# Optimization experiments

Hardware: AMD Instinct MI355X
Metric: run time of the kernel (lower is better)

The kernel has to match this reference:

```python
import jax, jax.numpy as jnp
import numpy as np

S = 4  # MC samples


def _gat_layer(x, mask, w, a_src, a_dst, bias):
    # x: (b,n,fin)  w: (H,fin,fout)  mask: (b,n,n) bool
    h = jnp.einsum('bnf,hfo->bhno', x, w)                      # (b,H,n,fout)
    th = jnp.tanh(h)
    att_src = jnp.einsum('bhno,ho->bhn', th, a_src)
    att_dst = jnp.einsum('bhno,ho->bhn', th, a_dst)
    logits = jax.nn.leaky_relu(att_src[:, :, :, None] + att_dst[:, :, None, :], 0.2)
    logits = jnp.where(mask[:, None, :, :], logits, jnp.float32(-1e9))
    att = jax.nn.softmax(logits, axis=-1)                      # (b,H,n,n)
    out = jnp.einsum('bhij,bhjo->bhio', att, h) + bias         # (b,H,n,fout)
    return out, att


def setup_inputs() -> dict:
    key = jax.random.key(0)
    ks = jax.random.split(key, 11)
    b, n, f0, emb_d = 128, 128, 64, 64
    H1, f1, H2, f2 = 8, 16, 1, 2
    fin1 = f0 + emb_d            # 128 (n_units[0] += 64)
    fin2 = H1 * f1               # 128 (heads concatenated between layers)
    x = jax.random.normal(ks[0], (b, n, f0), jnp.float32)
    emb = jax.random.normal(ks[1], (b, n, emb_d), jnp.float32)
    adj = jax.random.randint(ks[2], (b, n, n), 0, 2).astype(jnp.int32)
    adj = jnp.maximum(adj, jnp.eye(n, dtype=jnp.int32)[None])  # self-loops keep softmax rows valid
    w1 = jax.random.normal(ks[3], (S, H1, fin1, f1), jnp.float32) * 0.1
    a_src1 = jax.random.normal(ks[4], (S, H1, f1), jnp.float32) * 0.1
    a_dst1 = jax.random.normal(ks[5], (S, H1, f1), jnp.float32) * 0.1
    b1 = jax.random.normal(ks[6], (f1,), jnp.float32) * 0.1
    w2 = jax.random.normal(ks[7], (S, H2, fin2, f2), jnp.float32) * 0.1
    a_src2 = jax.random.normal(ks[8], (S, H2, f2), jnp.float32) * 0.1
    a_dst2 = jax.random.normal(ks[9], (S, H2, f2), jnp.float32) * 0.1
    b2 = jax.random.normal(ks[10], (f2,), jnp.float32) * 0.1
    return dict(x=x, emb=emb, adj=adj, w1=w1, a_src1=a_src1, a_dst1=a_dst1, b1=b1,
                w2=w2, a_src2=a_src2, a_dst2=a_dst2, b2=b2)


def reference(x, emb, adj, w1, a_src1, a_dst1, b1, w2, a_src2, a_dst2, b2):
    mask = adj.astype(bool)
    x0 = jnp.concatenate([x, emb], axis=-1)                    # (b,n,128)
    b, n = x0.shape[0], x0.shape[1]
    xs = jnp.broadcast_to(x0, (S,) + x0.shape)                 # same input for each MC sample
    layer = jax.vmap(_gat_layer, in_axes=(0, None, 0, 0, 0, None))
    # layer 1 (per-sample variational weights), ELU activation
    h1, att1 = layer(xs, mask, w1, a_src1, a_dst1, b1)         # h1: (S,b,H1,n,f1)
    h1 = jax.nn.elu(h1)
    # concat heads: transpose(1,2).view(bs,n,-1)
    xs2 = jnp.transpose(h1, (0, 1, 3, 2, 4)).reshape(S, b, n, -1)
    # layer 2 (last layer): no activation, mean over heads
    h2, att2 = layer(xs2, mask, w2, a_src2, a_dst2, b2)        # (S,b,1,n,2)
    out = h2.mean(axis=2)                                      # (S,b,n,2)
    logp = jax.nn.log_softmax(out, axis=-1)[:, :, -1, :]       # (S,b,2) -> ego node
    result = jnp.mean(logp, axis=0)                            # var_mean -> mean (return_uncertainty=False)
    return result
```

## Files before the change

### kernel.cpp

```cpp
#include <hip/hip_runtime.h>
#include <stdint.h>
#include <math.h>

typedef __attribute__((ext_vector_type(8))) short short8;
typedef __attribute__((ext_vector_type(4))) float floatx4;

#define L_HF    0
#define L_SRC   16384
#define L_DST   18432
#define L_MASK  20480
#define L_H2P   22528
#define L_SIZE  26624

union F8 { short8 s8; uint32_t u[4]; };

#if __has_builtin(__builtin_amdgcn_exp2f)
#define EXP2F __builtin_amdgcn_exp2f
#else
#define EXP2F exp2f
#endif
#define LOG2E 1.4426950408889634f

__device__ __forceinline__ uint32_t packbf(float a, float b){
  uint32_t ua = __float_as_uint(a), ub = __float_as_uint(b);
  uint32_t ra = (ua + 0x7fffu + ((ua>>16)&1u)) >> 16;
  uint32_t rb = (ub + 0x7fffu + ((ub>>16)&1u)) >> 16;
  return ra | (rb<<16);
}
__device__ __forceinline__ uint32_t packbf_t(float a, float b){
  return __builtin_amdgcn_perm(__float_as_uint(b), __float_as_uint(a), 0x07060302u);
}
__device__ __forceinline__ float fast_tanh(float x){
  float e = __expf(2.f*x);
  return 1.f - 2.f*__builtin_amdgcn_rcpf(e + 1.f);
}
__device__ __forceinline__ float red16(float x){
  x += __int_as_float(__builtin_amdgcn_update_dpp(0, __float_as_int(x), 0x128, 0xf, 0xf, true));
  x += __int_as_float(__builtin_amdgcn_update_dpp(0, __float_as_int(x), 0x124, 0xf, 0xf, true));
  x += __int_as_float(__builtin_amdgcn_update_dpp(0, __float_as_int(x), 0x122, 0xf, 0xf, true));
  x += __int_as_float(__builtin_amdgcn_update_dpp(0, __float_as_int(x), 0x121, 0xf, 0xf, true));
  return x;
}

__global__ __launch_bounds__(512,8) void gat_fused(
    const float* __restrict__ x,  const float* __restrict__ emb,
    const int* __restrict__ adj,  const float* __restrict__ w1,
    const float* __restrict__ a_src1, const float* __restrict__ a_dst1,
    const float* __restrict__ b1, const float* __restrict__ w2,
    float* __restrict__ ws_h2)
{
  __shared__ __align__(16) char smem[L_SIZE];
  char*     hf    = smem + L_HF;
  uint32_t* hf_u  = (uint32_t*)(smem + L_HF);
  float*    src_l = (float*)(smem + L_SRC);
  float*    dst_l = (float*)(smem + L_DST);
  uint32_t* mask_l= (uint32_t*)(smem + L_MASK);
  const uint4* mask4 = (const uint4*)(smem + L_MASK);
  float2*   h2p   = (float2*)(smem + L_H2P);

  const int t    = threadIdx.x;
  const int blk  = blockIdx.x;
  const int s    = blk >> 8;
  const int bb   = (blk & 255) >> 1;
  const int half = blk & 1;
  const int lane = t & 63, w = t >> 6;
  const int of = lane & 15, kg = lane >> 4;

  const int arow = w*16 + of;
  const float* xrow = x   + ((size_t)bb*128 + arow)*64;
  const float* erow = emb + ((size_t)bb*128 + arow)*64;
  short8 af[4];
  #pragma unroll
  for (int ks=0; ks<4; ++ks){
    int k = ks*32 + kg*8;
    const float* p = (k<64) ? (xrow+k) : (erow + (k-64));
    float4 f0 = *(const float4*)p, f1 = *(const float4*)(p+4);
    F8 fr;
    fr.u[0]=packbf(f0.x,f0.y); fr.u[1]=packbf(f0.z,f0.w);
    fr.u[2]=packbf(f1.x,f1.y); fr.u[3]=packbf(f1.z,f1.w);
    af[ks]=fr.s8;
  }

  {
    const float* w1s = w1 + (size_t)s*16384 + half*8192;
    #pragma unroll
    for (int r=0; r<2; ++r){
      int q = t + r*512;
      int ql = q & 63, ks = (q>>6)&3, ct = q>>8;
      const float* wp = w1s + ct*2048 + (ks*32 + (ql>>4)*8)*16 + (ql&15);
      F8 fr;
      fr.u[0]=packbf(wp[0],  wp[16]);
      fr.u[1]=packbf(wp[32], wp[48]);
      fr.u[2]=packbf(wp[64], wp[80]);
      fr.u[3]=packbf(wp[96], wp[112]);
      *(short8*)(hf + ((ct*4+ks)*64 + ql)*16) = fr.s8;
    }
  }

  {
    const int* adjb = adj + (size_t)bb*16384;
    #pragma unroll 4
    for (int rr=0; rr<16; ++rr){
      const int row = w*16 + rr;
      const int* ar = adjb + row*128;
      uint64_t m0 = __ballot(ar[lane] != 0);
      uint64_t m1 = __ballot(ar[64+lane] != 0);
      if (lane == 0)
        ((uint4*)mask_l)[row] = make_uint4((uint32_t)m0,(uint32_t)(m0>>32),
                                           (uint32_t)m1,(uint32_t)(m1>>32));
    }
  }
  __syncthreads();

  floatx4 acc[4];
  #pragma unroll
  for (int ct=0; ct<4; ++ct) acc[ct]=(floatx4){0.f,0.f,0.f,0.f};
  #pragma unroll
  for (int ct=0; ct<4; ++ct)
    #pragma unroll
    for (int ks=0; ks<4; ++ks){
      short8 bfr = *(const short8*)(hf + ((ct*4+ks)*64 + lane)*16);
      acc[ct] = __builtin_amdgcn_mfma_f32_16x16x32_bf16(af[ks], bfr, acc[ct], 0,0,0);
    }
  __syncthreads();

  const int ks_h = w>>1, kgp = (w&1)*2 + (kg>>1), vv = (kg&1)*2;
  #pragma unroll
  for (int ct=0; ct<4; ++ct){
    const int ghd = half*4 + ct;
    float asv = a_src1[s*128 + ghd*16 + of] * LOG2E;
    float adv = a_dst1[s*128 + ghd*16 + of] * LOG2E;
    float ps[4], pd[4];
    #pragma unroll
    for (int r=0; r<4; ++r){
      float th = fast_tanh(acc[ct][r]);
      ps[r] = red16(th*asv); pd[r] = red16(th*adv);
    }
    if (of==0){
      #pragma unroll
      for (int r=0; r<4; ++r){
        int i = w*16 + kg*4 + r;
        src_l[ct*128+i]=ps[r]; dst_l[ct*128+i]=pd[r];
      }
    }
    uint32_t p0 = packbf(acc[ct][0], acc[ct][1]);
    uint32_t p1 = packbf(acc[ct][2], acc[ct][3]);
    uint32_t* dsth = hf_u + ((ct*4+ks_h)*64 + kgp*16 + of)*4 + vv;
    *(uint2*)dsth = make_uint2(p0, p1);
  }
  __syncthreads();

  const int lhd = w >> 1;
  const int ghd = half*4 + lhd;
  const int rtb = (w&1)*4;
  float b1v  = b1[of];
  float w2c0 = w2[s*256 + (ghd*16+of)*2 + 0];
  float w2c1 = w2[s*256 + (ghd*16+of)*2 + 1];
  short8 hb[4];
  #pragma unroll
  for (int ks=0; ks<4; ++ks)
    hb[ks] = *(const short8*)(hf + ((lhd*4+ks)*64 + lane)*16);

  #pragma unroll
  for (int rtl=0; rtl<4; ++rtl){
    const int rt = rtb + rtl;
    const int im = rt*16 + of;
    float srcv = src_l[lhd*128 + im];
    uint4 mrow = mask4[im];
    floatx4 acc2 = (floatx4){0.f,0.f,0.f,0.f};
    float zp = 0.f;
    #pragma unroll
    for (int ks=0; ks<4; ++ks){
      const float* dp = dst_l + lhd*128 + ks*32 + kg*8;
      float4 d0 = *(const float4*)dp, d1 = *(const float4*)(dp+4);
      uint32_t mw = (ks==0)?mrow.x:(ks==1)?mrow.y:(ks==2)?mrow.z:mrow.w;
      uint32_t mbyte = mw >> (kg*8);
      float dj[8] = {d0.x,d0.y,d0.z,d0.w,d1.x,d1.y,d1.z,d1.w};
      float e[8];
      #pragma unroll
      for (int jj=0; jj<8; ++jj){
        float t0 = srcv + dj[jj];
        float lr = fmaxf(t0, 0.2f*t0);
        float ev = EXP2F(lr);
        ev = ((mbyte>>jj)&1u) ? ev : 0.f;
        e[jj]=ev; zp += ev;
      }
      F8 fr;
      fr.u[0]=packbf_t(e[0],e[1]); fr.u[1]=packbf_t(e[2],e[3]);
      fr.u[2]=packbf_t(e[4],e[5]); fr.u[3]=packbf_t(e[6],e[7]);
      acc2 = __builtin_amdgcn_mfma_f32_16x16x32_bf16(fr.s8, hb[ks], acc2, 0,0,0);
    }
    float zr = zp + __shfl_xor(zp,16); zr += __shfl_xor(zr,32);
    float zi = __builtin_amdgcn_rcpf(zr);
    float pc0[4], pc1[4];
    #pragma unroll
    for (int r=0; r<4; ++r){
      float ziR = __shfl(zi, kg*4+r);
      float o  = fmaf(acc2[r], ziR, b1v);
      float oe = (o>0.f) ? o : (__expf(o)-1.f);
      pc0[r] = red16(oe*w2c0);
      pc1[r] = red16(oe*w2c1);
    }
    if (of==0){
      #pragma unroll
      for (int r=0; r<4; ++r){
        int i = rt*16 + kg*4 + r;
        h2p[lhd*128 + i] = make_float2(pc0[r], pc1[r]);
      }
    }
  }
  __syncthreads();

  if (t < 256){
    const int jn = t>>1, cc = t&1;
    float hv = 0.f;
    #pragma unroll
    for (int hd2=0; hd2<4; ++hd2){
      float2 p = h2p[hd2*128+jn];
      hv += cc ? p.y : p.x;
    }
    ws_h2[(size_t)blk*256 + t] = hv;
  }
}

__global__ __launch_bounds__(256) void gat_tail(
    const float* __restrict__ ws_h2, const int* __restrict__ adj,
    const float* __restrict__ a_src2, const float* __restrict__ a_dst2,
    const float* __restrict__ b2, float* __restrict__ out)
{
  __shared__ float d2_l[128];
  __shared__ float red[16];
  __shared__ float srcE;
  const int bb = blockIdx.x, t = threadIdx.x;
  const int jn = t>>1, cc = t&1, lane = t&63, w = t>>6;
  const uint32_t bit = (adj[((size_t)bb*128+127)*128 + jn] != 0) ? 1u : 0u;
  float acc0=0.f, acc1=0.f;
  for (int s=0; s<4; ++s){
    float hv = ws_h2[(size_t)(s*256 + bb*2 + 0)*256 + t]
             + ws_h2[(size_t)(s*256 + bb*2 + 1)*256 + t];
    float th2 = fast_tanh(hv);
    float ps2 = th2*a_src2[s*2+cc];
    float pd2 = th2*a_dst2[s*2+cc];
    ps2 += __shfl_xor(ps2,1);
    pd2 += __shfl_xor(pd2,1);
    if (s) __syncthreads();
    if (cc==0) d2_l[jn]=pd2;
    if (t==254) srcE=ps2;
    __syncthreads();
    float t0 = srcE + d2_l[jn];
    float lg = fmaxf(t0, 0.2f*t0);
    float v  = bit ? lg : -1e9f;
    float mloc = v;
    #pragma unroll
    for (int off=32; off>=1; off>>=1) mloc = fmaxf(mloc, __shfl_xor(mloc,off));
    if (lane==0) red[w]=mloc;
    __syncthreads();
    float M = fmaxf(fmaxf(red[0],red[1]), fmaxf(red[2],red[3]));
    float e2 = __expf(v-M);
    float vA = e2*hv;
    float vZ = (cc==0) ? e2 : 0.f;
    #pragma unroll
    for (int off=2; off<=32; off<<=1){ vA+=__shfl_xor(vA,off); vZ+=__shfl_xor(vZ,off); }
    if (lane==0){ red[4+w]=vA; red[12+w]=vZ; }
    if (lane==1){ red[8+w]=vA; }
    __syncthreads();
    if (t==0){
      float S0 = red[4]+red[5]+red[6]+red[7];
      float S1 = red[8]+red[9]+red[10]+red[11];
      float Z  = red[12]+red[13]+red[14]+red[15];
      float o0 = S0/Z + b2[0];
      float o1 = S1/Z + b2[1];
      float mm = fmaxf(o0,o1);
      float lse = mm + logf(__expf(o0-mm)+__expf(o1-mm));
      acc0 += 0.25f*(o0 - lse);
      acc1 += 0.25f*(o1 - lse);
    }
  }
  if (t==0){ out[bb*2+0]=acc0; out[bb*2+1]=acc1; }
}

extern "C" void kernel_launch(void* const* d_in, const int* in_sizes, int n_in,
                              void* d_out, int out_size, void* d_ws, size_t ws_size,
                              hipStream_t stream) {
  const float* x      = (const float*)d_in[0];
  const float* emb    = (const float*)d_in[1];
  const int*   adj    = (const int*)d_in[2];
  const float* w1     = (const float*)d_in[3];
  const float* a_src1 = (const float*)d_in[4];
  const float* a_dst1 = (const float*)d_in[5];
  const float* b1     = (const float*)d_in[6];
  const float* w2     = (const float*)d_in[7];
  const float* a_src2 = (const float*)d_in[8];
  const float* a_dst2 = (const float*)d_in[9];
  const float* b2     = (const float*)d_in[10];

  float* ws_h2 = (float*)d_ws;

  gat_fused<<<dim3(1024), dim3(512), 0, stream>>>(x, emb, adj, w1, a_src1, a_dst1,
                                                  b1, w2, ws_h2);
  gat_tail<<<dim3(128), dim3(256), 0, stream>>>(ws_h2, adj, a_src2, a_dst2, b2,
                                                (float*)d_out);
}
```

Measured before the change: 129.4 us.

## Fuse tail kernel into main kernel via last-block atomic counter

Removes the separate gat_tail launch. Each of the 8 blocks covering a batch element increments a per-batch atomic counter after a threadfence, and the last block to arrive computes the layer-2 attention, softmax and log-softmax for that batch. It reuses the ego-row adjacency mask already held in shared memory. This saves one kernel launch and its ramp-up, but adds a memset launch, a threadfence and atomic per block, and a serialized tail at the end of the final blocks.

```diff
diff --git a/kernel.cpp b/kernel.cpp
--- a/kernel.cpp
+++ b/kernel.cpp
@@ -12,6 +12,9 @@
 #define L_H2P   22528
 #define L_SIZE  26624
 
+#define WS_H2_FLOATS  (1024*256)
+#define WS_CNT_OFF    (WS_H2_FLOATS*4)
+
 union F8 { short8 s8; uint32_t u[4]; };
 
 #if __has_builtin(__builtin_amdgcn_exp2f)
@@ -47,9 +50,13 @@
     const int* __restrict__ adj,  const float* __restrict__ w1,
     const float* __restrict__ a_src1, const float* __restrict__ a_dst1,
     const float* __restrict__ b1, const float* __restrict__ w2,
-    float* __restrict__ ws_h2)
+    const float* __restrict__ a_src2, const float* __restrict__ a_dst2,
+    const float* __restrict__ b2,
+    float* __restrict__ ws_h2, uint32_t* __restrict__ cnt,
+    float* __restrict__ outp)
 {
   __shared__ __align__(16) char smem[L_SIZE];
+  __shared__ uint32_t s_last;
   char*     hf    = smem + L_HF;
   uint32_t* hf_u  = (uint32_t*)(smem + L_HF);
   float*    src_l = (float*)(smem + L_SRC);
@@ -221,62 +228,74 @@
     }
     ws_h2[(size_t)blk*256 + t] = hv;
   }
-}
-
-__global__ __launch_bounds__(256) void gat_tail(
-    const float* __restrict__ ws_h2, const int* __restrict__ adj,
-    const float* __restrict__ a_src2, const float* __restrict__ a_dst2,
-    const float* __restrict__ b2, float* __restrict__ out)
-{
-  __shared__ float d2_l[128];
-  __shared__ float red[16];
-  __shared__ float srcE;
-  const int bb = blockIdx.x, t = threadIdx.x;
-  const int jn = t>>1, cc = t&1, lane = t&63, w = t>>6;
-  const uint32_t bit = (adj[((size_t)bb*128+127)*128 + jn] != 0) ? 1u : 0u;
-  float acc0=0.f, acc1=0.f;
-  for (int s=0; s<4; ++s){
-    float hv = ws_h2[(size_t)(s*256 + bb*2 + 0)*256 + t]
-             + ws_h2[(size_t)(s*256 + bb*2 + 1)*256 + t];
-    float th2 = fast_tanh(hv);
-    float ps2 = th2*a_src2[s*2+cc];
-    float pd2 = th2*a_dst2[s*2+cc];
-    ps2 += __shfl_xor(ps2,1);
-    pd2 += __shfl_xor(pd2,1);
-    if (s) __syncthreads();
-    if (cc==0) d2_l[jn]=pd2;
-    if (t==254) srcE=ps2;
-    __syncthreads();
-    float t0 = srcE + d2_l[jn];
-    float lg = fmaxf(t0, 0.2f*t0);
-    float v  = bit ? lg : -1e9f;
-    float mloc = v;
-    #pragma unroll
-    for (int off=32; off>=1; off>>=1) mloc = fmaxf(mloc, __shfl_xor(mloc,off));
-    if (lane==0) red[w]=mloc;
-    __syncthreads();
-    float M = fmaxf(fmaxf(red[0],red[1]), fmaxf(red[2],red[3]));
-    float e2 = __expf(v-M);
-    float vA = e2*hv;
-    float vZ = (cc==0) ? e2 : 0.f;
-    #pragma unroll
-    for (int off=2; off<=32; off<<=1){ vA+=__shfl_xor(vA,off); vZ+=__shfl_xor(vZ,off); }
-    if (lane==0){ red[4+w]=vA; red[12+w]=vZ; }
-    if (lane==1){ red[8+w]=vA; }
-    __syncthreads();
-    if (t==0){
-      float S0 = red[4]+red[5]+red[6]+red[7];
-      float S1 = red[8]+red[9]+red[10]+red[11];
-      float Z  = red[12]+red[13]+red[14]+red[15];
-      float o0 = S0/Z + b2[0];
-      float o1 = S1/Z + b2[1];
-      float mm = fmaxf(o0,o1);
-      float lse = mm + logf(__expf(o0-mm)+__expf(o1-mm));
-      acc0 += 0.25f*(o0 - lse);
-      acc1 += 0.25f*(o1 - lse);
-    }
-  }
-  if (t==0){ out[bb*2+0]=acc0; out[bb*2+1]=acc1; }
+
+  __threadfence();
+  __syncthreads();
+  if (t==0) s_last = (atomicAdd(&cnt[bb], 1u) == 7u) ? 1u : 0u;
+  __syncthreads();
+  if (!s_last) return;
+  __threadfence();
+
+  {
+    float* d2_l = (float*)(smem + L_H2P);
+    float* red  = (float*)(smem + L_H2P + 512);
+    float* srcE = (float*)(smem + L_H2P + 576);
+    const int jn = t>>1, cc = t&1;
+    const bool act = (t<256);
+    uint32_t bit = 0;
+    if (act) bit = (mask_l[127*4 + (jn>>5)] >> (jn&31)) & 1u;
+    float acc0=0.f, acc1=0.f;
+    for (int ss=0; ss<4; ++ss){
+      float hv=0.f, ps2=0.f, pd2=0.f;
+      if (act){
+        hv = ws_h2[(size_t)(ss*256 + bb*2 + 0)*256 + t]
+           + ws_h2[(size_t)(ss*256 + bb*2 + 1)*256 + t];
+        float th2 = fast_tanh(hv);
+        ps2 = th2*a_src2[ss*2+cc];
+        pd2 = th2*a_dst2[ss*2+cc];
+        ps2 += __shfl_xor(ps2,1);
+        pd2 += __shfl_xor(pd2,1);
+      }
+      if (ss) __syncthreads();
+      if (act){
+        if (cc==0) d2_l[jn]=pd2;
+        if (t==254) *srcE=ps2;
+      }
+      __syncthreads();
+      float v = -1e9f;
+      if (act){
+        float t0 = *srcE + d2_l[jn];
+        float lg = fmaxf(t0, 0.2f*t0);
+        v = bit ? lg : -1e9f;
+      }
+      float mloc = v;
+      #pragma unroll
+      for (int off=32; off>=1; off>>=1) mloc = fmaxf(mloc, __shfl_xor(mloc,off));
+      if (act && lane==0) red[w]=mloc;
+      __syncthreads();
+      float M = fmaxf(fmaxf(red[0],red[1]), fmaxf(red[2],red[3]));
+      float e2 = act ? __expf(v-M) : 0.f;
+      float vA = e2*hv;
+      float vZ = (act && cc==0) ? e2 : 0.f;
+      #pragma unroll
+      for (int off=2; off<=32; off<<=1){ vA+=__shfl_xor(vA,off); vZ+=__shfl_xor(vZ,off); }
+      if (act && lane==0){ red[4+w]=vA; red[12+w]=vZ; }
+      if (act && lane==1){ red[8+w]=vA; }
+      __syncthreads();
+      if (t==0){
+        float S0 = red[4]+red[5]+red[6]+red[7];
+        float S1 = red[8]+red[9]+red[10]+red[11];
+        float Z  = red[12]+red[13]+red[14]+red[15];
+        float o0 = S0/Z + b2[0];
+        float o1 = S1/Z + b2[1];
+        float mm = fmaxf(o0,o1);
+        float lse = mm + logf(__expf(o0-mm)+__expf(o1-mm));
+        acc0 += 0.25f*(o0 - lse);
+        acc1 += 0.25f*(o1 - lse);
+      }
+    }
+    if (t==0){ outp[bb*2+0]=acc0; outp[bb*2+1]=acc1; }
+  }
 }
 
 extern "C" void kernel_launch(void* const* d_in, const int* in_sizes, int n_in,
@@ -294,10 +313,11 @@
   const float* a_dst2 = (const float*)d_in[9];
   const float* b2     = (const float*)d_in[10];
 
-  float* ws_h2 = (float*)d_ws;
-
+  float*    ws_h2 = (float*)d_ws;
+  uint32_t* cnt   = (uint32_t*)((char*)d_ws + WS_CNT_OFF);
+
+  hipMemsetAsync(cnt, 0, 128*sizeof(uint32_t), stream);
   gat_fused<<<dim3(1024), dim3(512), 0, stream>>>(x, emb, adj, w1, a_src1, a_dst1,
-                                                  b1, w2, ws_h2);
-  gat_tail<<<dim3(128), dim3(256), 0, stream>>>(ws_h2, adj, a_src2, a_dst2, b2,
-                                                (float*)d_out);
-}
+                                                  b1, w2, a_src2, a_dst2, b2,
+                                                  ws_h2, cnt, (float*)d_out);
+}
```

Measured after the change: 259.5 us. +100.5%, slower.
